# Kernel tuning notes

Measured on AMD Instinct MI355X. Metric: run time of the kernel, lower is better.

## Reference

```python
import jax, jax.numpy as jnp
import numpy as np

N_HEAD = 16
D_MODEL = 1024
B, C = 4, 2048

def setup_inputs() -> dict:
    key = jax.random.key(0)
    k_x, k_wq, k_bq, k_wo, k_bo = jax.random.split(key, 5)
    s = 0.02
    return {
        "x": jax.random.normal(k_x, (B, C, D_MODEL), dtype=jnp.float32),
        "W_qkv": jax.random.normal(k_wq, (D_MODEL, 3 * D_MODEL), dtype=jnp.float32) * s,
        "b_qkv": jax.random.normal(k_bq, (3 * D_MODEL,), dtype=jnp.float32) * s,
        "W_o": jax.random.normal(k_wo, (D_MODEL, D_MODEL), dtype=jnp.float32) * s,
        "b_o": jax.random.normal(k_bo, (D_MODEL,), dtype=jnp.float32) * s,
    }

def reference(x, W_qkv, b_qkv, W_o, b_o):
    Bsz, Cq, D = x.shape
    H = N_HEAD
    hd = D // H
    qkv = x @ W_qkv + b_qkv                      # [B,C,3D]
    Q, K, V = jnp.split(qkv, 3, axis=2)
    # [B,C,H,hd] -> [B,H,C,hd]
    Q = Q.reshape(Bsz, Cq, H, hd).transpose(0, 2, 1, 3)
    K = K.reshape(Bsz, Cq, H, hd).transpose(0, 2, 1, 3)
    V = V.reshape(Bsz, Cq, H, hd).transpose(0, 2, 1, 3)
    scale = 1.0 / np.sqrt(hd).astype(np.float32)
    att = jnp.einsum('bhqd,bhkd->bhqk', Q, K) * scale
    causal = jnp.tril(jnp.ones((Cq, Cq), dtype=bool))
    att = jnp.where(causal, att, jnp.float32(-jnp.inf))
    att = jax.nn.softmax(att, axis=-1)           # dropout = identity (eval)
    out = jnp.einsum('bhqk,bhkd->bhqd', att, V)  # [B,H,C,hd]
    out = out.transpose(0, 2, 1, 3).reshape(Bsz, Cq, D)
    return out @ W_o + b_o
```

## Files before the change

### kernel.cpp

```cpp
#include <hip/hip_runtime.h>
#include <hip/hip_bf16.h>

typedef __attribute__((ext_vector_type(8))) short bf16x8;
typedef __attribute__((ext_vector_type(4))) float f32x4;

#define NH 16
#define DM 1024
#define HD 64
#define CSEQ 2048
#define MROWS 8192
#define NBH 64

static __device__ __forceinline__ unsigned short f2bf(float f) {
  __hip_bfloat16 h = __float2bfloat16(f);
  return *reinterpret_cast<unsigned short*>(&h);
}

static __device__ __forceinline__ short bf_qscale(short s) {
  unsigned u = ((unsigned)(unsigned short)s) << 16;
  float f = __builtin_bit_cast(float, u) * 0.18033688f;
  return (short)f2bf(f);
}

static __device__ __forceinline__ void gload_lds16(const void* g, void* l) {
  __builtin_amdgcn_global_load_lds(
      (const __attribute__((address_space(1))) unsigned int*)g,
      (__attribute__((address_space(3))) unsigned int*)l, 16, 0, 0);
}

__global__ __launch_bounds__(256) void cast_f32_bf16(const float* __restrict__ in,
                                                     unsigned short* __restrict__ out,
                                                     int n4) {
  int stride = gridDim.x * blockDim.x;
  for (int i = blockIdx.x * blockDim.x + threadIdx.x; i < n4; i += stride) {
    float4 v = ((const float4*)in)[i];
    ushort4 o;
    o.x = f2bf(v.x); o.y = f2bf(v.y); o.z = f2bf(v.z); o.w = f2bf(v.w);
    ((ushort4*)out)[i] = o;
  }
}

__global__ __launch_bounds__(256) void transpose_cast(const float* __restrict__ src,
                                                      unsigned short* __restrict__ dst,
                                                      int K, int N) {
  __shared__ float tile[32][33];
  int tx = threadIdx.x, ty = threadIdx.y;
  int n0 = blockIdx.x * 32, k0 = blockIdx.y * 32;
  #pragma unroll
  for (int i = 0; i < 32; i += 8)
    tile[ty + i][tx] = src[(size_t)(k0 + ty + i) * N + n0 + tx];
  __syncthreads();
  #pragma unroll
  for (int i = 0; i < 32; i += 8)
    dst[(size_t)(n0 + ty + i) * K + k0 + tx] = f2bf(tile[tx][ty + i]);
}

template<int MODE>
__global__ __launch_bounds__(256) void gemm128(const unsigned short* __restrict__ A,
                                               const unsigned short* __restrict__ BT,
                                               const float* __restrict__ bias,
                                               float* __restrict__ outF,
                                               unsigned short* __restrict__ outQKV,
                                               int N, int K) {
  __shared__ char sAb[2][8192];
  __shared__ char sBb[2][8192];
  int tid = threadIdx.x;
  int w = tid >> 6, l = tid & 63, g = l >> 4, cx = l & 15;
  int bm = blockIdx.y * 128, bn = blockIdx.x * 128;
  int wm = (w >> 1) * 64, wn = (w & 1) * 64;

  f32x4 acc[4][4];
  #pragma unroll
  for (int mi = 0; mi < 4; mi++)
    #pragma unroll
    for (int ni = 0; ni < 4; ni++)
      acc[mi][ni] = (f32x4){0.f, 0.f, 0.f, 0.f};

  for (int kk = 0; kk < K; kk += 64) {
    __syncthreads();
    #pragma unroll
    for (int s = 0; s < 2; s++) {
      #pragma unroll
      for (int c2 = 0; c2 < 2; c2++) {
        int c = tid + c2 * 256;
        int row = c >> 2, sp = c & 3, sl = sp ^ ((row >> 1) & 3);
        gload_lds16(A + (size_t)(bm + row) * K + kk + s * 32 + sl * 8, sAb[s] + c * 16);
        gload_lds16(BT + (size_t)(bn + row) * K + kk + s * 32 + sl * 8, sBb[s] + c * 16);
      }
    }
    __syncthreads();

    #pragma unroll
    for (int s = 0; s < 2; s++) {
      bf16x8 af[4], bfr[4];
      #pragma unroll
      for (int mi = 0; mi < 4; mi++) {
        int row = wm + mi * 16 + cx;
        af[mi] = *(const bf16x8*)(sAb[s] + row * 64 + ((g ^ ((row >> 1) & 3)) << 4));
      }
      #pragma unroll
      for (int ni = 0; ni < 4; ni++) {
        int row = wn + ni * 16 + cx;
        bfr[ni] = *(const bf16x8*)(sBb[s] + row * 64 + ((g ^ ((row >> 1) & 3)) << 4));
      }
      #pragma unroll
      for (int mi = 0; mi < 4; mi++)
        #pragma unroll
        for (int ni = 0; ni < 4; ni++)
          acc[mi][ni] = __builtin_amdgcn_mfma_f32_16x16x32_bf16(af[mi], bfr[ni], acc[mi][ni], 0, 0, 0);
    }
  }

  #pragma unroll
  for (int mi = 0; mi < 4; mi++) {
    #pragma unroll
    for (int ni = 0; ni < 4; ni++) {
      int col = bn + wn + ni * 16 + cx;
      float bv = bias[col];
      int row0 = bm + wm + mi * 16 + g * 4;
      #pragma unroll
      for (int r = 0; r < 4; r++) {
        float v = acc[mi][ni][r] + bv;
        int rr = row0 + r;
        if (MODE == 0) {
          outF[(size_t)rr * N + col] = v;
        } else {
          int which = col >> 10, rem = col & 1023;
          int h = rem >> 6, d = rem & 63;
          int b = rr >> 11, cq = rr & 2047;
          if (which == 2) {
            int pos = (cq & ~31) + (((cq >> 2) & 3) << 3) + (((cq >> 4) & 1) << 2) + (cq & 3);
            outQKV[((size_t)2 * NBH + b * NH + h) * (CSEQ * HD) +
                   (size_t)d * CSEQ + pos] = f2bf(v);
          } else {
            outQKV[((size_t)which * NBH + b * NH + h) * (CSEQ * HD) + (size_t)cq * HD + d] = f2bf(v);
          }
        }
      }
    }
  }
}

__global__ __launch_bounds__(512, 4) void attn_kernel(const unsigned short* __restrict__ Qb,
                                                      const unsigned short* __restrict__ Kb,
                                                      const unsigned short* __restrict__ VTb,
                                                      unsigned short* __restrict__ O) {
  __shared__ char sKb[2][16384];
  __shared__ char sVt[2][16384];
  int tid = threadIdx.x;
  int w = tid >> 6, l = tid & 63, g = l >> 4, cx = l & 15;
  int gid = blockIdx.x;
  int bh = ((gid >> 7) << 3) | (gid & 7);
  int qt = 15 - ((gid >> 3) & 15);

  const unsigned short* Qp  = Qb  + (size_t)bh * CSEQ * HD;
  const unsigned short* Kp  = Kb  + (size_t)bh * CSEQ * HD;
  const unsigned short* VTp = VTb + (size_t)bh * CSEQ * HD;

  int qrow = qt * 128 + w * 16 + cx;
  bf16x8 qf[2];
  qf[0] = *(const bf16x8*)(Qp + (size_t)qrow * HD + g * 8);
  qf[1] = *(const bf16x8*)(Qp + (size_t)qrow * HD + 32 + g * 8);
  #pragma unroll
  for (int kc = 0; kc < 2; kc++)
    #pragma unroll
    for (int j = 0; j < 8; j++) qf[kc][j] = bf_qscale(qf[kc][j]);

  f32x4 o[4];
  #pragma unroll
  for (int nf2 = 0; nf2 < 4; nf2++) o[nf2] = (f32x4){0.f, 0.f, 0.f, 0.f};
  float mrow = -INFINITY, lrow = 0.f;

  int c0 = tid, c1 = tid + 512;
  int krow0 = c0 >> 3, ksl0 = (c0 & 7) ^ (krow0 & 7);
  int krow1 = c1 >> 3, ksl1 = (c1 & 7) ^ (krow1 & 7);
  int vd0 = c0 >> 4, vsl0 = (c0 & 15) ^ (vd0 & 7);
  int vd1 = c1 >> 4, vsl1 = (c1 & 15) ^ (vd1 & 7);
  const unsigned short* Ksrc0 = Kp + (size_t)krow0 * HD + ksl0 * 8;
  const unsigned short* Ksrc1 = Kp + (size_t)krow1 * HD + ksl1 * 8;
  const unsigned short* Vsrc0 = VTp + (size_t)vd0 * CSEQ + vsl0 * 8;
  const unsigned short* Vsrc1 = VTp + (size_t)vd1 * CSEQ + vsl1 * 8;

  gload_lds16(Ksrc0, sKb[0] + c0 * 16);
  gload_lds16(Ksrc1, sKb[0] + c1 * 16);
  gload_lds16(Vsrc0, sVt[0] + c0 * 16);
  gload_lds16(Vsrc1, sVt[0] + c1 * 16);
  __syncthreads();
  int cur = 0;

  for (int kt = 0; kt <= qt; kt++) {
    if (kt < qt) {
      size_t ko = (size_t)(kt + 1) * 128 * HD;
      size_t vo = (size_t)(kt + 1) * 128;
      gload_lds16(Ksrc0 + ko, sKb[cur ^ 1] + c0 * 16);
      gload_lds16(Ksrc1 + ko, sKb[cur ^ 1] + c1 * 16);
      gload_lds16(Vsrc0 + vo, sVt[cur ^ 1] + c0 * 16);
      gload_lds16(Vsrc1 + vo, sVt[cur ^ 1] + c1 * 16);
    }
    const char* Kc = sKb[cur];
    const char* Vc = sVt[cur];

    f32x4 sacc[8];
    #pragma unroll
    for (int nf = 0; nf < 8; nf++) sacc[nf] = (f32x4){0.f, 0.f, 0.f, 0.f};
    __builtin_amdgcn_s_setprio(1);
    #pragma unroll
    for (int kc = 0; kc < 2; kc++) {
      #pragma unroll
      for (int nf = 0; nf < 8; nf++) {
        int row = nf * 16 + cx;
        bf16x8 kf = *(const bf16x8*)(Kc + row * 128 + ((((kc << 2) | g) ^ (row & 7)) << 4));
        sacc[nf] = __builtin_amdgcn_mfma_f32_16x16x32_bf16(kf, qf[kc], sacc[nf], 0, 0, 0);
      }
    }
    __builtin_amdgcn_s_setprio(0);

    if (kt == qt) {
      #pragma unroll
      for (int nf = 0; nf < 8; nf++)
        #pragma unroll
        for (int r = 0; r < 4; r++)
          if (nf * 16 + 4 * g + r > w * 16 + cx) sacc[nf][r] = -INFINITY;
    }
    float m8[8];
    #pragma unroll
    for (int nf = 0; nf < 8; nf++)
      m8[nf] = fmaxf(fmaxf(sacc[nf][0], sacc[nf][1]), fmaxf(sacc[nf][2], sacc[nf][3]));
    float mx = fmaxf(fmaxf(fmaxf(m8[0], m8[1]), fmaxf(m8[2], m8[3])),
                     fmaxf(fmaxf(m8[4], m8[5]), fmaxf(m8[6], m8[7])));
    mx = fmaxf(mx, __shfl_xor(mx, 16));
    mx = fmaxf(mx, __shfl_xor(mx, 32));

    if (!__all(mx - mrow <= 8.f)) {
      float mnew = fmaxf(mrow, mx);
      float alpha = __builtin_amdgcn_exp2f(mrow - mnew);
      mrow = mnew;
      lrow *= alpha;
      #pragma unroll
      for (int r = 0; r < 4; r++) {
        float ar = __shfl(alpha, (l & 48) | ((l >> 2) & 12) | r);
        #pragma unroll
        for (int nf2 = 0; nf2 < 4; nf2++) o[nf2][r] *= ar;
      }
    }
    #pragma unroll
    for (int nf = 0; nf < 8; nf++)
      #pragma unroll
      for (int r = 0; r < 4; r++)
        sacc[nf][r] = __builtin_amdgcn_exp2f(sacc[nf][r] - mrow);
    float s8[8];
    #pragma unroll
    for (int nf = 0; nf < 8; nf++)
      s8[nf] = (sacc[nf][0] + sacc[nf][1]) + (sacc[nf][2] + sacc[nf][3]);
    float sum = ((s8[0] + s8[1]) + (s8[2] + s8[3])) + ((s8[4] + s8[5]) + (s8[6] + s8[7]));
    sum += __shfl_xor(sum, 16);
    sum += __shfl_xor(sum, 32);
    lrow += sum;

    bf16x8 pa[4];
    #pragma unroll
    for (int kc = 0; kc < 4; kc++) {
      #pragma unroll
      for (int j = 0; j < 4; j++) {
        pa[kc][j]     = (short)f2bf(sacc[2 * kc][j]);
        pa[kc][j + 4] = (short)f2bf(sacc[2 * kc + 1][j]);
      }
    }

    __builtin_amdgcn_s_setprio(1);
    #pragma unroll
    for (int kc = 0; kc < 4; kc++) {
      #pragma unroll
      for (int nf2 = 0; nf2 < 4; nf2++) {
        int d = nf2 * 16 + cx;
        bf16x8 vf = *(const bf16x8*)(Vc + ((d * 256 + (((kc << 2) | g) << 4)) ^ ((d & 7) << 4)));
        o[nf2] = __builtin_amdgcn_mfma_f32_16x16x32_bf16(pa[kc], vf, o[nf2], 0, 0, 0);
      }
    }
    __builtin_amdgcn_s_setprio(0);

    if (kt < qt) {
      __syncthreads();
      cur ^= 1;
    }
  }

  int b = bh >> 4, h = bh & 15;
  float linv = 1.0f / lrow;
  #pragma unroll
  for (int r = 0; r < 4; r++) {
    float inv = __shfl(linv, (l & 48) | ((l >> 2) & 12) | r);
    int q = qt * 128 + w * 16 + 4 * g + r;
    size_t base = ((size_t)(b * CSEQ + q)) * DM + h * HD;
    #pragma unroll
    for (int nf2 = 0; nf2 < 4; nf2++)
      O[base + nf2 * 16 + cx] = f2bf(o[nf2][r] * inv);
  }
}

extern "C" void kernel_launch(void* const* d_in, const int* in_sizes, int n_in,
                              void* d_out, int out_size, void* d_ws, size_t ws_size,
                              hipStream_t stream) {
  const float* x    = (const float*)d_in[0];
  const float* Wqkv = (const float*)d_in[1];
  const float* bqkv = (const float*)d_in[2];
  const float* Wo   = (const float*)d_in[3];
  const float* bo   = (const float*)d_in[4];
  float* out = (float*)d_out;

  unsigned short* ws = (unsigned short*)d_ws;
  const size_t XB_OFF    = 0;
  const size_t WQKVT_OFF = 8388608;
  const size_t WOT_OFF   = WQKVT_OFF + 3145728;
  const size_t QKV_OFF   = WOT_OFF + 1048576;
  const size_t ATT_OFF   = QKV_OFF + 3 * 8388608;

  unsigned short* xb    = ws + XB_OFF;
  unsigned short* wqkvT = ws + WQKVT_OFF;
  unsigned short* woT   = ws + WOT_OFF;
  unsigned short* qkv   = ws + QKV_OFF;
  unsigned short* att   = ws + ATT_OFF;

  cast_f32_bf16<<<2048, 256, 0, stream>>>(x, xb, (MROWS * DM) / 4);
  transpose_cast<<<dim3(3 * DM / 32, DM / 32), dim3(32, 8), 0, stream>>>(Wqkv, wqkvT, DM, 3 * DM);
  transpose_cast<<<dim3(DM / 32, DM / 32), dim3(32, 8), 0, stream>>>(Wo, woT, DM, DM);

  gemm128<1><<<dim3(3 * DM / 128, MROWS / 128), 256, 0, stream>>>(
      xb, wqkvT, bqkv, nullptr, qkv, 3 * DM, DM);

  attn_kernel<<<dim3(1024), 512, 0, stream>>>(
      qkv, qkv + 8388608, qkv + 16777216, att);

  gemm128<0><<<dim3(DM / 128, MROWS / 128), 256, 0, stream>>>(
      att, woT, bo, out, nullptr, DM, DM);
}
```

Before: 215.7 us.

## Replace 128x128 GEMM with 256x256 eight-wave pipelined GEMM kernel

Rewrites both projection GEMMs to use 256x256 tiles with 512 threads, a larger XOR-swizzled LDS layout, and an interleaved schedule that issues global-to-LDS prefetch for the next K-step between quarter-tile MFMA phases. It also remaps block indices for L2 locality and raises wave priority around MFMA bursts. The aim is higher MFMA utilisation and hidden load latency, at the cost of 128KB of LDS per block and fewer blocks (the output projection gets only 128 blocks), which may underfill the GPU.

```diff
diff --git a/kernel.cpp b/kernel.cpp
--- a/kernel.cpp
+++ b/kernel.cpp
@@ -55,72 +55,140 @@
     dst[(size_t)(n0 + ty + i) * K + k0 + tx] = f2bf(tile[tx][ty + i]);
 }
 
+
+static __device__ __forceinline__ void stage_half(const unsigned short* s0,
+                                                  const unsigned short* s1,
+                                                  char* dst, int c0, int c1) {
+  gload_lds16(s0, dst + c0 * 16);
+  gload_lds16(s1, dst + c1 * 16);
+}
+
+template<int CNT>
+static __device__ __forceinline__ void ld_frags(const char* base, int r0, int cx, int g,
+                                                bf16x8 (*out)[2]) {
+  #pragma unroll
+  for (int i = 0; i < CNT; i++) {
+    int row = r0 + i * 16 + cx;
+    #pragma unroll
+    for (int kc = 0; kc < 2; kc++)
+      out[i][kc] = *(const bf16x8*)(base + row * 128 + ((((kc << 2) | g) ^ (row & 7)) << 4));
+  }
+}
+
+static __device__ __forceinline__ void mfma_q(const bf16x8 af[4][2], const bf16x8 bfr[2][2],
+                                              f32x4 acc[8][4], int qm, int qn) {
+  #pragma unroll
+  for (int kc = 0; kc < 2; kc++)
+    #pragma unroll
+    for (int mi = 0; mi < 4; mi++)
+      #pragma unroll
+      for (int ni = 0; ni < 2; ni++)
+        acc[qm * 4 + mi][qn * 2 + ni] = __builtin_amdgcn_mfma_f32_16x16x32_bf16(
+            af[mi][kc], bfr[ni][kc], acc[qm * 4 + mi][qn * 2 + ni], 0, 0, 0);
+}
+
+#define BARR() __builtin_amdgcn_s_barrier()
+#define LGKM0() asm volatile("s_waitcnt lgkmcnt(0)" ::: "memory")
+#define PRIO1() __builtin_amdgcn_s_setprio(1)
+#define PRIO0() __builtin_amdgcn_s_setprio(0)
+
 template<int MODE>
-__global__ __launch_bounds__(256) void gemm128(const unsigned short* __restrict__ A,
-                                               const unsigned short* __restrict__ BT,
-                                               const float* __restrict__ bias,
-                                               float* __restrict__ outF,
-                                               unsigned short* __restrict__ outQKV,
-                                               int N, int K) {
-  __shared__ char sAb[2][8192];
-  __shared__ char sBb[2][8192];
+__global__ __launch_bounds__(512, 2) void gemm256(const unsigned short* __restrict__ A,
+                                                  const unsigned short* __restrict__ BT,
+                                                  const float* __restrict__ bias,
+                                                  float* __restrict__ outF,
+                                                  unsigned short* __restrict__ outQKV,
+                                                  int N, int K) {
+  __shared__ char sA[2][32768];
+  __shared__ char sB[2][32768];
   int tid = threadIdx.x;
   int w = tid >> 6, l = tid & 63, g = l >> 4, cx = l & 15;
-  int bm = blockIdx.y * 128, bn = blockIdx.x * 128;
-  int wm = (w >> 1) * 64, wn = (w & 1) * 64;
-
-  f32x4 acc[4][4];
-  #pragma unroll
-  for (int mi = 0; mi < 4; mi++)
-    #pragma unroll
-    for (int ni = 0; ni < 4; ni++)
-      acc[mi][ni] = (f32x4){0.f, 0.f, 0.f, 0.f};
-
-  for (int kk = 0; kk < K; kk += 64) {
-    __syncthreads();
-    #pragma unroll
-    for (int s = 0; s < 2; s++) {
-      #pragma unroll
-      for (int c2 = 0; c2 < 2; c2++) {
-        int c = tid + c2 * 256;
-        int row = c >> 2, sp = c & 3, sl = sp ^ ((row >> 1) & 3);
-        gload_lds16(A + (size_t)(bm + row) * K + kk + s * 32 + sl * 8, sAb[s] + c * 16);
-        gload_lds16(BT + (size_t)(bn + row) * K + kk + s * 32 + sl * 8, sBb[s] + c * 16);
-      }
-    }
-    __syncthreads();
-
-    #pragma unroll
-    for (int s = 0; s < 2; s++) {
-      bf16x8 af[4], bfr[4];
-      #pragma unroll
-      for (int mi = 0; mi < 4; mi++) {
-        int row = wm + mi * 16 + cx;
-        af[mi] = *(const bf16x8*)(sAb[s] + row * 64 + ((g ^ ((row >> 1) & 3)) << 4));
-      }
-      #pragma unroll
-      for (int ni = 0; ni < 4; ni++) {
-        int row = wn + ni * 16 + cx;
-        bfr[ni] = *(const bf16x8*)(sBb[s] + row * 64 + ((g ^ ((row >> 1) & 3)) << 4));
-      }
-      #pragma unroll
-      for (int mi = 0; mi < 4; mi++)
-        #pragma unroll
-        for (int ni = 0; ni < 4; ni++)
-          acc[mi][ni] = __builtin_amdgcn_mfma_f32_16x16x32_bf16(af[mi], bfr[ni], acc[mi][ni], 0, 0, 0);
-    }
-  }
-
-  #pragma unroll
-  for (int mi = 0; mi < 4; mi++) {
-    #pragma unroll
-    for (int ni = 0; ni < 4; ni++) {
-      int col = bn + wn + ni * 16 + cx;
+  int wm = (w >> 2) * 128, wn = (w & 3) * 64;
+
+  int nwgx = gridDim.x;
+  int nwg = nwgx * gridDim.y;
+  int gid = blockIdx.y * nwgx + blockIdx.x;
+  int swz = (gid & 7) * (nwg >> 3) + (gid >> 3);
+  int bm = (swz / nwgx) * 256, bn = (swz % nwgx) * 256;
+
+  int c0 = tid, c1 = tid + 512;
+  int ar0 = c0 >> 3, as0 = ((c0 & 7) ^ (ar0 & 7)) * 8;
+  int ar1 = c1 >> 3, as1 = ((c1 & 7) ^ (ar1 & 7)) * 8;
+  const unsigned short* Ap0 = A + (size_t)(bm + ar0) * K + as0;
+  const unsigned short* Ap1 = A + (size_t)(bm + ar1) * K + as1;
+  const unsigned short* Bp0 = BT + (size_t)(bn + ar0) * K + as0;
+  const unsigned short* Bp1 = BT + (size_t)(bn + ar1) * K + as1;
+  const size_t HS = (size_t)128 * K;
+
+  f32x4 acc[8][4];
+  #pragma unroll
+  for (int i = 0; i < 8; i++)
+    #pragma unroll
+    for (int j = 0; j < 4; j++) acc[i][j] = (f32x4){0.f, 0.f, 0.f, 0.f};
+
+  int NT = K >> 6;
+
+  stage_half(Ap0,      Ap1,      sA[0],         c0, c1);
+  stage_half(Ap0 + HS, Ap1 + HS, sA[0] + 16384, c0, c1);
+  stage_half(Bp0,      Bp1,      sB[0],         c0, c1);
+  stage_half(Bp0 + HS, Bp1 + HS, sB[0] + 16384, c0, c1);
+  stage_half(Ap0 + 64, Ap1 + 64, sA[1],         c0, c1);
+  asm volatile("s_waitcnt vmcnt(2)" ::: "memory");
+  BARR();
+
+  int cur = 0;
+  for (int t = 0; t < NT; t++) {
+    const char* Ac = sA[cur];
+    const char* Bc = sB[cur];
+    char* An = sA[cur ^ 1];
+    char* Bn = sB[cur ^ 1];
+    int kn  = (t + 1) << 6;
+    int kn2 = (t + 2) << 6;
+    bool h1 = (t + 1) < NT, h2 = (t + 2) < NT;
+    bf16x8 af[4][2], bfr[2][2];
+
+    ld_frags<4>(Ac, wm, cx, g, af);
+    ld_frags<2>(Bc, wn, cx, g, bfr);
+    if (h1) stage_half(Ap0 + HS + kn, Ap1 + HS + kn, An + 16384, c0, c1);
+    BARR(); LGKM0();
+    PRIO1(); mfma_q(af, bfr, acc, 0, 0); PRIO0();
+    BARR();
+
+    ld_frags<2>(Bc, wn + 32, cx, g, bfr);
+    if (h1) stage_half(Bp0 + kn, Bp1 + kn, Bn, c0, c1);
+    BARR(); LGKM0();
+    PRIO1(); mfma_q(af, bfr, acc, 0, 1); PRIO0();
+    BARR();
+
+    ld_frags<4>(Ac, wm + 64, cx, g, af);
+    ld_frags<2>(Bc, wn, cx, g, bfr);
+    if (h1) stage_half(Bp0 + HS + kn, Bp1 + HS + kn, Bn + 16384, c0, c1);
+    BARR(); LGKM0();
+    PRIO1(); mfma_q(af, bfr, acc, 1, 0); PRIO0();
+    BARR();
+
+    ld_frags<2>(Bc, wn + 32, cx, g, bfr);
+    BARR(); LGKM0();
+    if (h2) stage_half(Ap0 + kn2, Ap1 + kn2, sA[cur], c0, c1);
+    PRIO1(); mfma_q(af, bfr, acc, 1, 1); PRIO0();
+    if (h1) {
+      if (h2) { asm volatile("s_waitcnt vmcnt(2)" ::: "memory"); }
+      else    { asm volatile("s_waitcnt vmcnt(0)" ::: "memory"); }
+    }
+    BARR();
+    cur ^= 1;
+  }
+
+  #pragma unroll
+  for (int ai = 0; ai < 8; ai++) {
+    #pragma unroll
+    for (int aj = 0; aj < 4; aj++) {
+      int col = bn + wn + aj * 16 + cx;
       float bv = bias[col];
-      int row0 = bm + wm + mi * 16 + g * 4;
+      int row0 = bm + wm + ai * 16 + g * 4;
       #pragma unroll
       for (int r = 0; r < 4; r++) {
-        float v = acc[mi][ni][r] + bv;
+        float v = acc[ai][aj][r] + bv;
         int rr = row0 + r;
         if (MODE == 0) {
           outF[(size_t)rr * N + col] = v;
@@ -325,12 +393,12 @@
   transpose_cast<<<dim3(3 * DM / 32, DM / 32), dim3(32, 8), 0, stream>>>(Wqkv, wqkvT, DM, 3 * DM);
   transpose_cast<<<dim3(DM / 32, DM / 32), dim3(32, 8), 0, stream>>>(Wo, woT, DM, DM);
 
-  gemm128<1><<<dim3(3 * DM / 128, MROWS / 128), 256, 0, stream>>>(
+  gemm256<1><<<dim3(3 * DM / 256, MROWS / 256), 512, 0, stream>>>(
       xb, wqkvT, bqkv, nullptr, qkv, 3 * DM, DM);
 
   attn_kernel<<<dim3(1024), 512, 0, stream>>>(
       qkv, qkv + 8388608, qkv + 16777216, att);
 
-  gemm128<0><<<dim3(DM / 128, MROWS / 128), 256, 0, stream>>>(
+  gemm256<0><<<dim3(DM / 256, MROWS / 256), 512, 0, stream>>>(
       att, woT, bo, out, nullptr, DM, DM);
 }
```

Result: slower. 225.0 us (+4.3%).
